# Performance work log

Measured on AMD Instinct MI355X. Metric: run time of the kernel, lower is better.

## Reference

```python
import jax, jax.numpy as jnp
import numpy as np

N = 64
K_CHEB = 5
EPS = 1e-5

# db4 decomposition filters (scaling_filter.mat Lo_D / Hi_D, length 8)
_LO = np.array([-0.010597401784997278, 0.032883011666982945, 0.030841381835986965,
                -0.18703481171888114, -0.02798376941698385, 0.6308807679295904,
                0.7148465705525415, 0.23037781330885523], dtype=np.float32)
_HI = np.array([-0.23037781330885523, 0.7148465705525415, -0.6308807679295904,
                -0.02798376941698385, 0.18703481171888114, 0.030841381835986965,
                0.032883011666982945, -0.010597401784997278], dtype=np.float32)
# torch stores np.flip(filters) and Conv2d does cross-correlation -> use flipped taps here too
_KERN = np.stack([_LO[::-1], _HI[::-1]])[:, None, None, :].copy()  # [2,1,1,8]


def _wavelet_step(x):
    # x: [B, C, 1, W]; circular pad 3 each side, depthwise len-8 conv, stride 2
    p = 3  # filter_length // 2 - 1
    xp = jnp.concatenate([x[..., -p:], x, x[..., :p]], axis=-1)
    b, c, h, wp = xp.shape
    out = jax.lax.conv_general_dilated(
        xp.reshape(b * c, 1, h, wp), jnp.asarray(_KERN), (1, 2), 'VALID',
        dimension_numbers=('NCHW', 'OIHW', 'NCHW'))
    out = out.reshape(b, c, 2, h, -1)
    return out[:, :, 0], out[:, :, 1]  # (approx, detail)


def _cbam(x, fc1, fc2, sa_w):
    # x: [B, 657, 1, 64]; channel attention then spatial attention
    def mlp(v):  # v: [B, C, 1, 1]
        h = jax.nn.relu(jnp.einsum('oc,bchw->bohw', fc1, v))
        return jnp.einsum('oc,bchw->bohw', fc2, h)
    avg = x.mean(axis=(2, 3), keepdims=True)
    mx = x.max(axis=(2, 3), keepdims=True)
    x = x * jax.nn.sigmoid(mlp(avg) + mlp(mx))
    s = jnp.concatenate([x.mean(axis=1, keepdims=True), x.max(axis=1, keepdims=True)], axis=1)
    sa = jax.nn.sigmoid(jax.lax.conv_general_dilated(
        s, sa_w, (1, 1), ((3, 3), (3, 3)), dimension_numbers=('NCHW', 'OIHW', 'NCHW')))
    return x * sa


def _global_edge_weight(w_tril, mask):
    xs, ys = np.tril_indices(N)
    E = jnp.zeros((N, N), w_tril.dtype).at[xs, ys].set(w_tril)
    E = E + E.T - jnp.diag(jnp.diag(E))
    return (E * mask).reshape(-1)


def _norm_adj(edges, w):
    # PyG NewSGConv.norm: add remaining self-loops (fill=1), deg from |w|, sym normalize
    row, col = edges[0], edges[1]
    has_self = jnp.zeros((N,), w.dtype).at[row].add(jnp.where(row == col, 1.0, 0.0)) > 0
    w_self = jnp.where(has_self, 0.0, 1.0).astype(w.dtype)
    deg = jnp.zeros((N,), w.dtype).at[row].add(jnp.abs(w)) + w_self
    dsafe = jnp.where(deg > 0, deg, 1.0)
    dinv = jnp.where(deg > 0, jax.lax.rsqrt(dsafe), 0.0)
    norm = dinv[row] * w * dinv[col]
    A = jnp.zeros((N, N), w.dtype).at[col, row].add(norm)  # out[i] = sum_j A[i,j] x[j]
    return A + jnp.diag(dinv * w_self * dinv)


def _gcn_block(x, A, W, b, g, be):
    # x: [B, N, C_in]; K-hop SGConv propagation, linear, train-mode batchnorm over (B, N)
    for _ in range(K_CHEB):
        x = jnp.einsum('ij,bjc->bic', A, x)
    x = x @ W.T + b
    mean = x.mean(axis=(0, 1))
    var = x.var(axis=(0, 1))
    return (x - mean) * jax.lax.rsqrt(var + EPS) * g + be


def _classify(x, W1, b1, g, be, W2, b2):
    out = x.reshape(x.shape[0], -1) @ W1.T + b1
    out = (out - out.mean(0)) * jax.lax.rsqrt(out.var(0) + EPS) * g + be
    return jax.nn.log_softmax(out @ W2.T + b2, axis=1)


def _forward(x, local_graph_weight, global_mask, ca_fc1, ca_fc2, sa_conv, edge_weight_tril,
             ld_W, ld_b, ld_g, ld_be, ld1_W, ld1_b, ld1_g, ld1_be,
             d_W, d_b, d_g, d_be, d1_W, d1_b, d1_g, d1_be,
             cls_W1, cls_b1, cls_g, cls_be, cls_W2, cls_b2, edges):
    xc = jnp.transpose(x, (0, 3, 2, 1))        # [B, 657, 1, 64]
    xc = _cbam(xc, ca_fc1, ca_fc2, sa_conv)
    xh = jnp.transpose(xc, (0, 3, 2, 1))       # [B, 64, 1, 657]
    # fi = floor(log2(200)) = 7 -> 4 decomposition levels: 657->328->164->82->41
    out1, _gamma = _wavelet_step(xh)
    out2, _beta = _wavelet_step(out1)
    out3, _alpha = _wavelet_step(out2)
    delta, _theta = _wavelet_step(out3)        # [B, 64, 1, 41]
    delta = delta[:, :, 0, :]                  # squeeze -> [B, 64, 41]
    gw = _global_edge_weight(edge_weight_tril, global_mask)
    A_loc = _norm_adj(edges, local_graph_weight)
    A_glb = _norm_adj(edges, gw)
    lf = _gcn_block(delta, A_loc, ld_W, ld_b, ld_g, ld_be)
    lf = _gcn_block(lf, A_loc, ld1_W, ld1_b, ld1_g, ld1_be)
    gf = _gcn_block(delta, A_glb, d_W, d_b, d_g, d_be)
    gf = _gcn_block(gf, A_glb, d1_W, d1_b, d1_g, d1_be)
    feat = jnp.concatenate([lf.mean(-1, keepdims=True), gf.mean(-1, keepdims=True)], axis=2)  # [B,64,2]
    return _classify(feat, cls_W1, cls_b1, cls_g, cls_be, cls_W2, cls_b2)


def setup_inputs() -> dict:
    key = jax.random.key(0)
    ks = iter(jax.random.split(key, 16))
    B = 512
    f32 = jnp.float32
    def rn(shape, s=0.05):
        return jax.random.normal(next(ks), shape, f32) * s
    ii = jnp.arange(N, dtype=jnp.int32)
    edges = jnp.stack([jnp.repeat(ii, N), jnp.tile(ii, N)])  # full 64x64 mesh (incl. self loops)
    return dict(
        x=jax.random.normal(next(ks), (B, N, 1, 657), f32),
        local_graph_weight=jax.random.uniform(next(ks), (N * N,), f32),
        global_mask=jnp.ones((N, N), f32),
        ca_fc1=rn((82, 657)),
        ca_fc2=rn((657, 82)),
        sa_conv=rn((1, 2, 7, 7), 0.1),
        edge_weight_tril=jax.random.uniform(next(ks), (N * (N + 1) // 2,), f32),
        ld_W=rn((16, 41)), ld_b=jnp.zeros(16, f32), ld_g=jnp.ones(16, f32), ld_be=jnp.zeros(16, f32),
        ld1_W=rn((4, 16)), ld1_b=jnp.zeros(4, f32), ld1_g=jnp.ones(4, f32), ld1_be=jnp.zeros(4, f32),
        d_W=rn((16, 41)), d_b=jnp.zeros(16, f32), d_g=jnp.ones(16, f32), d_be=jnp.zeros(16, f32),
        d1_W=rn((4, 16)), d1_b=jnp.zeros(4, f32), d1_g=jnp.ones(4, f32), d1_be=jnp.zeros(4, f32),
        cls_W1=rn((32, 128)), cls_b1=jnp.zeros(32, f32), cls_g=jnp.ones(32, f32), cls_be=jnp.zeros(32, f32),
        cls_W2=rn((2, 32)), cls_b2=jnp.zeros(2, f32),
        edges=edges,
    )


def reference(x, local_graph_weight, global_mask, ca_fc1, ca_fc2, sa_conv, edge_weight_tril,
              ld_W, ld_b, ld_g, ld_be, ld1_W, ld1_b, ld1_g, ld1_be,
              d_W, d_b, d_g, d_be, d1_W, d1_b, d1_g, d1_be,
              cls_W1, cls_b1, cls_g, cls_be, cls_W2, cls_b2, edges):
    return _forward(x, local_graph_weight, global_mask, ca_fc1, ca_fc2, sa_conv, edge_weight_tril,
                    ld_W, ld_b, ld_g, ld_be, ld1_W, ld1_b, ld1_g, ld1_be,
                    d_W, d_b, d_g, d_be, d1_W, d1_b, d1_g, d1_be,
                    cls_W1, cls_b1, cls_g, cls_be, cls_W2, cls_b2, edges)
```

## Files before the change

kernel.cpp:

```cpp
#include <hip/hip_runtime.h>
#include <math.h>

#define NB 512
#define NN 64
#define TL 657
#define LV1 328
#define LV2 164
#define LV3 82
#define LV4 41
#define HID 82
#define ST 66
#define NGB 32

#define WS_M      0
#define WS_ACC    32768
#define WS_SMEAN  36864
#define WS_SMAX   167936
#define WS_CSP    299008
#define WS_CMP    2990080
#define WS_CATT   5681152
#define WS_DELTA  299008
#define WS_Y1     5681152
#define WS_Y2     299008
#define WS_OUT1   1347584

#define ACC_Y1 0
#define ACC_Y2 64
#define ACC_O1 80

__device__ __forceinline__ float sigmoidf_(float v){ return 1.0f/(1.0f+expf(-v)); }

__device__ __forceinline__ void wav_level(float* __restrict__ dst, const float* __restrict__ src,
                                          int outL, int inL, int lane){
  const float DLO[8] = {0.23037781330885523f, 0.7148465705525415f, 0.6308807679295904f,
                        -0.02798376941698385f, -0.18703481171888114f, 0.030841381835986965f,
                        0.032883011666982945f, -0.010597401784997278f};
  for (int k=lane; k<outL; k+=64){
    int i0 = 2*k - 3;
    float a = 0.f;
    #pragma unroll
    for (int j=0;j<8;j++){
      int idx = i0 + j;
      idx = (idx < 0) ? idx + inL : ((idx >= inL) ? idx - inL : idx);
      a += src[idx]*DLO[j];
    }
    dst[k] = a;
  }
}

__global__ __launch_bounds__(512) void k_stats(
    const float* __restrict__ x,
    const float* __restrict__ lgw, const float* __restrict__ gmask,
    const float* __restrict__ tril, const int* __restrict__ edges,
    float* __restrict__ csum_p, float* __restrict__ cmax_p,
    float* __restrict__ Mout, double* __restrict__ acc)
{
  __shared__ float smem[8848];
  __shared__ float deg[64], hsv[64], dinv[64], wself[64];
  int tid = threadIdx.x;
  int bid = blockIdx.x;

  if (bid < NGB){
    int g  = bid >> 4;
    int s4 = (bid & 15) * 4;
    float* Wbuf = smem;
    float* Amat = smem + 4096;
    float* Rc   = smem + 8320;
    float* Rn   = smem + 8584;
    if (bid==0 && tid<512) acc[tid]=0.0;
    for (int e=tid;e<4096;e+=512){
      float w;
      if (g==0) w = lgw[e];
      else {
        int i=e>>6, j=e&63;
        int aa = (i>j)? i:j, bb = (i>j)? j:i;
        w = tril[aa*(aa+1)/2 + bb] * gmask[e];
      }
      Wbuf[e] = w;
    }
    for (int i=tid;i<NN*ST;i+=512) Amat[i] = 0.f;
    if (tid<64){ deg[tid]=0.f; hsv[tid]=0.f; }
    __syncthreads();
    {
      int e0 = tid*8;
      int runr = edges[e0];
      float runv = 0.f;
      #pragma unroll
      for (int i=0;i<8;i++){
        int e = e0+i;
        int r = edges[e];
        int c = edges[4096+e];
        float w = Wbuf[e];
        if (r != runr){ atomicAdd(&deg[runr], runv); runr = r; runv = 0.f; }
        runv += fabsf(w);
        if (r == c) hsv[r] = 1.f;
      }
      atomicAdd(&deg[runr], runv);
    }
    __syncthreads();
    if (tid<64){
      float w_ = (hsv[tid] > 0.f) ? 0.f : 1.f;
      float d = deg[tid] + w_;
      dinv[tid] = (d > 0.f) ? rsqrtf(d) : 0.f;
      wself[tid] = w_;
    }
    __syncthreads();
    for (int e=tid;e<4096;e+=512){
      int r = edges[e], c = edges[4096+e];
      float nm = dinv[r]*Wbuf[e]*dinv[c];
      atomicAdd(&Amat[c*ST+r], nm);
    }
    __syncthreads();
    if (tid<64) Amat[tid*ST+tid] += dinv[tid]*wself[tid]*dinv[tid];
    __syncthreads();
    if (tid < 256){
      int r = tid>>6, c = tid&63;
      Rc[r*ST+c] = Amat[(s4+r)*ST+c];
    }
    __syncthreads();
    #pragma unroll
    for (int it=0; it<4; it++){
      if (tid < 256){
        int r = tid>>6, c = tid&63;
        const float* rr = &Rc[r*ST];
        float a0=0.f, a1=0.f;
        #pragma unroll 8
        for (int k=0;k<64;k+=2){
          a0 += rr[k]  *Amat[k*ST+c];
          a1 += rr[k+1]*Amat[(k+1)*ST+c];
        }
        Rn[r*ST+c] = a0+a1;
      }
      __syncthreads();
      float* t = Rc; Rc = Rn; Rn = t;
    }
    if (tid < 256){
      int r = tid>>6, c = tid&63;
      Mout[g*4096 + (s4+r)*64 + c] = Rc[r*ST+c];
    }
    return;
  }

  int sid = bid - NGB;
  int b = sid >> 1, split = sid & 1;
  const float4* xb4 = (const float4*)(x + (size_t)b*NN*TL) + (size_t)split*8*657;
  int f0 = tid;
  int f1 = 512 + tid;
  bool has1 = (f1 < 657);
  float4 S0 = make_float4(0.f,0.f,0.f,0.f);
  float4 M0 = make_float4(-INFINITY,-INFINITY,-INFINITY,-INFINITY);
  float4 S1 = S0, M1 = M0;
  #pragma unroll
  for (int g=0; g<8; ++g){
    float4 v = xb4[g*657 + f0];
    S0.x += v.x; S0.y += v.y; S0.z += v.z; S0.w += v.w;
    M0.x = fmaxf(M0.x, v.x); M0.y = fmaxf(M0.y, v.y);
    M0.z = fmaxf(M0.z, v.z); M0.w = fmaxf(M0.w, v.w);
    if (has1){
      float4 w = xb4[g*657 + f1];
      S1.x += w.x; S1.y += w.y; S1.z += w.z; S1.w += w.w;
      M1.x = fmaxf(M1.x, w.x); M1.y = fmaxf(M1.y, w.y);
      M1.z = fmaxf(M1.z, w.z); M1.w = fmaxf(M1.w, w.w);
    }
  }
  float* Sf = smem;
  float* Mf = smem + 2628;
  *(float4*)&Sf[4*f0] = S0;
  *(float4*)&Mf[4*f0] = M0;
  if (has1){
    *(float4*)&Sf[4*f1] = S1;
    *(float4*)&Mf[4*f1] = M1;
  }
  __syncthreads();
  for (int c=tid; c<TL; c+=512){
    float s = (Sf[c] + Sf[c+657]) + (Sf[c+1314] + Sf[c+1971]);
    float m = fmaxf(fmaxf(Mf[c], Mf[c+657]), fmaxf(Mf[c+1314], Mf[c+1971]));
    csum_p[(size_t)sid*TL + c] = s;
    cmax_p[(size_t)sid*TL + c] = m;
  }
}

__global__ __launch_bounds__(512) void k_mlp(
    const float* __restrict__ csum_p, const float* __restrict__ cmax_p,
    const float* __restrict__ fc1, const float* __restrict__ fc2,
    float* __restrict__ catt_g)
{
  __shared__ float cs[660], cm[660], h[84];
  int tid = threadIdx.x, b = blockIdx.x;
  int wv = tid>>6, lane = tid&63;
  const float* s0 = csum_p + (size_t)(2*b  )*TL;
  const float* s1 = csum_p + (size_t)(2*b+1)*TL;
  const float* m0 = cmax_p + (size_t)(2*b  )*TL;
  const float* m1 = cmax_p + (size_t)(2*b+1)*TL;
  for (int c=tid; c<TL; c+=512){
    cs[c] = s0[c] + s1[c];
    cm[c] = fmaxf(m0[c], m1[c]);
  }
  __syncthreads();
  for (int o=wv; o<HID; o+=8){
    const float* fr = fc1 + (size_t)o*TL;
    float a = 0.f, bm = 0.f;
    #pragma unroll
    for (int i=0;i<11;i++){
      int c = lane + 64*i;
      if (c < TL){
        float f = fr[c];
        a += f*cs[c]; bm += f*cm[c];
      }
    }
    #pragma unroll
    for (int off=32;off;off>>=1){
      a  += __shfl_xor(a,off);
      bm += __shfl_xor(bm,off);
    }
    if (lane==0)
      h[o] = fmaxf(a*(1.0f/64.0f),0.f) + fmaxf(bm,0.f);
  }
  __syncthreads();
  for (int c=tid; c<TL; c+=512){
    const float2* fr = (const float2*)(fc2 + (size_t)c*HID);
    float a0=0.f, a1=0.f;
    #pragma unroll
    for (int u2=0;u2<41;u2++){
      float2 v = fr[u2];
      a0 += v.x*h[2*u2]; a1 += v.y*h[2*u2+1];
    }
    catt_g[(size_t)b*TL + c] = sigmoidf_(a0+a1);
  }
}

__global__ __launch_bounds__(256) void k_wav(
    const float* __restrict__ x, const float* __restrict__ catt_g,
    float* __restrict__ delta, float* __restrict__ smean, float* __restrict__ smax)
{
  __shared__ float catt[660];
  __shared__ float buf[2664];
  __shared__ float o1b[4][332];
  __shared__ float o2b[4][166];
  __shared__ float o3b[4][84];
  int tid = threadIdx.x, b = blockIdx.x, q = blockIdx.y;
  for (int i=tid;i<TL;i+=256) catt[i] = catt_g[(size_t)b*TL + i];
  __syncthreads();
  const float4* g4 = (const float4*)(x + ((size_t)b*NN + q*4)*TL);
  for (int f=tid; f<657; f+=256){
    float4 v = g4[f];
    int e = 4*f;
    if (f==164 || f==328 || f==492){
      float ev[4] = {v.x, v.y, v.z, v.w};
      #pragma unroll
      for (int j=0;j<4;j++){
        int ee = e+j;
        int r = (ee>=657) + (ee>=1314) + (ee>=1971);
        buf[ee + 12*r] = ev[j];
      }
    } else {
      int r = (e>=657) + (e>=1314) + (e>=1971);
      *(float4*)&buf[e + 12*r] = v;
    }
  }
  __syncthreads();
  int wv = tid>>6, lane = tid&63;
  int n = q*4 + wv;
  float* y = &buf[669*wv];
  float ls = 0.f, lm = -INFINITY;
  #pragma unroll
  for (int i=0;i<11;i++){
    int t = lane + 64*i;
    if (t < TL){
      float vv = y[t]*catt[t];
      y[t] = vv; ls += vv; lm = fmaxf(lm,vv);
    }
  }
  #pragma unroll
  for (int off=32;off;off>>=1){
    ls += __shfl_xor(ls,off);
    lm = fmaxf(lm, __shfl_xor(lm,off));
  }
  if (lane==0){ smean[b*NN+n] = ls*(1.0f/657.0f); smax[b*NN+n] = lm; }
  wav_level(o1b[wv], y,       LV1, TL,  lane);
  wav_level(o2b[wv], o1b[wv], LV2, LV1, lane);
  wav_level(o3b[wv], o2b[wv], LV3, LV2, lane);
  if (lane < LV4){
    const float DLO[8] = {0.23037781330885523f, 0.7148465705525415f, 0.6308807679295904f,
                          -0.02798376941698385f, -0.18703481171888114f, 0.030841381835986965f,
                          0.032883011666982945f, -0.010597401784997278f};
    int i0 = 2*lane - 3;
    float a = 0.f;
    #pragma unroll
    for (int j=0;j<8;j++){
      int idx = i0 + j;
      idx = (idx < 0) ? idx + LV3 : ((idx >= LV3) ? idx - LV3 : idx);
      a += o3b[wv][idx]*DLO[j];
    }
    delta[((size_t)b*NN + n)*LV4 + lane] = a;
  }
}

__global__ __launch_bounds__(256) void k_gcn1(
  const float* __restrict__ delta, const float* __restrict__ Mmat,
  const float* __restrict__ smean, const float* __restrict__ smax,
  const float* __restrict__ saw,
  const float* __restrict__ ldW, const float* __restrict__ ldb,
  const float* __restrict__ dW, const float* __restrict__ db2,
  float* __restrict__ Y1, double* __restrict__ acc)
{
  __shared__ float Dl[NN*LV4];
  __shared__ float Tt[NN*16];
  __shared__ float Mm[4096];
  __shared__ float Wl[16*LV4];
  __shared__ float satt[NN];
  __shared__ double red[256];
  int tid=threadIdx.x, b=blockIdx.x;
  if (tid < NN){
    float a = 0.f;
    #pragma unroll
    for (int kw=0;kw<7;kw++){
      int w = tid + kw - 3;
      if (0<=w && w<NN) a += smean[b*NN+w]*saw[21+kw] + smax[b*NN+w]*saw[70+kw];
    }
    satt[tid] = sigmoidf_(a);
  }
  __syncthreads();
  const float* ds = delta + (size_t)b*NN*LV4;
  for (int i=tid;i<NN*LV4;i+=256) Dl[i] = ds[i]*satt[i/LV4];
  for (int g=0; g<2; g++){
    const float* Ws = g ? dW : ldW;
    const float* bs = g ? db2 : ldb;
    for (int i=tid;i<16*LV4;i+=256) Wl[i]=Ws[i];
    const float4* Mm4 = (const float4*)(Mmat + g*4096);
    for (int i=tid;i<1024;i+=256) *(float4*)&Mm[4*i] = Mm4[i];
    __syncthreads();
    for (int e=tid;e<NN*16;e+=256){
      int n=e>>4, o=e&15;
      const float* dr=&Dl[n*LV4];
      const float* wr=&Wl[o*LV4];
      float a=0.f;
      #pragma unroll 8
      for (int c=0;c<LV4;c++) a += dr[c]*wr[c];
      Tt[e]=a;
    }
    __syncthreads();
    float bias = bs[tid&15];
    float ps=0.f, pq=0.f;
    for (int m=0;m<4;m++){
      int e=tid+256*m;
      int n=e>>4, o=e&15;
      float a=bias;
      #pragma unroll 8
      for (int k=0;k<64;k++) a += Mm[n*64+k]*Tt[k*16+o];
      Y1[((size_t)b*NN+n)*32 + g*16 + o] = a;
      ps += a; pq += a*a;
    }
    red[tid]=(double)ps;
    __syncthreads();
    if (tid<16){ double t=0; for (int r=tid;r<256;r+=16) t+=red[r]; atomicAdd(&acc[ACC_Y1+g*32+tid], t); }
    __syncthreads();
    red[tid]=(double)pq;
    __syncthreads();
    if (tid<16){ double t=0; for (int r=tid;r<256;r+=16) t+=red[r]; atomicAdd(&acc[ACC_Y1+g*32+16+tid], t); }
    __syncthreads();
  }
}

__global__ __launch_bounds__(256) void k_gcn2(
  const float* __restrict__ Y1, const float* __restrict__ Mmat,
  const float* __restrict__ ldg, const float* __restrict__ ldbe,
  const float* __restrict__ dg, const float* __restrict__ dbe,
  const float* __restrict__ ld1W, const float* __restrict__ ld1b,
  const float* __restrict__ d1W, const float* __restrict__ d1b,
  float* __restrict__ Y2, double* __restrict__ acc)
{
  __shared__ float Yl[NN*32];
  __shared__ float T2[NN*8];
  __shared__ float Mm[2*4096];
  __shared__ float scl[32], sht[32];
  __shared__ double red[256];
  int tid=threadIdx.x, b=blockIdx.x;
  const float4* ys4 = (const float4*)(Y1 + (size_t)b*NN*32);
  for (int i=tid;i<512;i+=256) *(float4*)&Yl[4*i] = ys4[i];
  const float4* Mm4 = (const float4*)Mmat;
  for (int i=tid;i<2048;i+=256) *(float4*)&Mm[4*i] = Mm4[i];
  if (tid<32){
    int g=tid>>4, o=tid&15;
    double s=acc[ACC_Y1+g*32+o], q=acc[ACC_Y1+g*32+16+o];
    double mean=s/32768.0;
    double var=q/32768.0 - mean*mean;
    float gam = g? dg[o] : ldg[o];
    float bet = g? dbe[o] : ldbe[o];
    float sc = gam * rsqrtf((float)var + 1e-5f);
    scl[tid]=sc; sht[tid]=bet - (float)mean*sc;
  }
  __syncthreads();
  for (int i=tid;i<NN*32;i+=256){ int c=i&31; Yl[i]=Yl[i]*scl[c]+sht[c]; }
  __syncthreads();
  for (int e=tid;e<NN*8;e+=256){
    int n=e>>3, c=e&7, g=c>>2, p=c&3;
    const float* w = (g? d1W : ld1W) + p*16;
    const float* yr = &Yl[n*32 + g*16];
    float a=0.f;
    #pragma unroll
    for (int o=0;o<16;o++) a += yr[o]*w[o];
    T2[e]=a;
  }
  __syncthreads();
  float ps=0.f,pq=0.f;
  for (int m=0;m<2;m++){
    int e=tid+256*m;
    int n=e>>3, c=e&7, g=c>>2;
    float a = g? d1b[c&3] : ld1b[c&3];
    const float* mr=&Mm[g*4096+n*64];
    #pragma unroll 8
    for (int k=0;k<64;k++) a += mr[k]*T2[k*8+c];
    Y2[((size_t)b*NN+n)*8 + c] = a;
    ps+=a; pq+=a*a;
  }
  red[tid]=(double)ps; __syncthreads();
  if (tid<8){ double t=0; for (int r=tid;r<256;r+=8) t+=red[r]; atomicAdd(&acc[ACC_Y2 + (tid>>2)*8 + (tid&3)], t); }
  __syncthreads();
  red[tid]=(double)pq; __syncthreads();
  if (tid<8){ double t=0; for (int r=tid;r<256;r+=8) t+=red[r]; atomicAdd(&acc[ACC_Y2 + (tid>>2)*8 + 4 + (tid&3)], t); }
}

__global__ __launch_bounds__(64) void k_featcls(
  const float* __restrict__ Y2,
  const float* __restrict__ ld1g, const float* __restrict__ ld1be,
  const float* __restrict__ d1g, const float* __restrict__ d1be,
  const float* __restrict__ W1, const float* __restrict__ b1,
  float* __restrict__ out1, double* __restrict__ acc)
{
  __shared__ float f[128];
  __shared__ float scl[8], sht[8];
  int tid=threadIdx.x, b=blockIdx.x;
  if (tid<8){
    int g=tid>>2, p=tid&3;
    double s=acc[ACC_Y2+g*8+p], q=acc[ACC_Y2+g*8+4+p];
    double mean=s/32768.0;
    double var=q/32768.0-mean*mean;
    float gam = g? d1g[p]:ld1g[p];
    float bet = g? d1be[p]:ld1be[p];
    float sc = gam*rsqrtf((float)var+1e-5f);
    scl[tid]=sc; sht[tid]=bet-(float)mean*sc;
  }
  __syncthreads();
  {
    const float* yr = Y2 + ((size_t)b*NN+tid)*8;
    float lf=0.f, gf=0.f;
    #pragma unroll
    for (int p=0;p<4;p++){
      lf += yr[p]*scl[p]+sht[p];
      gf += yr[4+p]*scl[4+p]+sht[4+p];
    }
    f[2*tid]   = lf*0.25f;
    f[2*tid+1] = gf*0.25f;
  }
  __syncthreads();
  if (tid<32){
    const float* w = W1 + tid*128;
    float a = b1[tid];
    #pragma unroll 4
    for (int m=0;m<128;m++) a += w[m]*f[m];
    out1[b*32+tid]=a;
    atomicAdd(&acc[ACC_O1+tid], (double)a);
    atomicAdd(&acc[ACC_O1+32+tid], (double)(a*a));
  }
}

__global__ __launch_bounds__(64) void k_cls2(
  const float* __restrict__ out1,
  const float* __restrict__ cg, const float* __restrict__ cbe,
  const float* __restrict__ W2, const float* __restrict__ b2,
  const double* __restrict__ acc, float* __restrict__ out)
{
  __shared__ float v[32];
  __shared__ float z[2];
  int tid=threadIdx.x, b=blockIdx.x;
  if (tid<32){
    double s=acc[ACC_O1+tid], q=acc[ACC_O1+32+tid];
    double mean=s/512.0;
    double var=q/512.0-mean*mean;
    float sc=cg[tid]*rsqrtf((float)var+1e-5f);
    float sh=cbe[tid]-(float)mean*sc;
    v[tid]=out1[b*32+tid]*sc+sh;
  }
  __syncthreads();
  if (tid<2){
    const float* w=W2+tid*32;
    float a=b2[tid];
    #pragma unroll
    for (int j=0;j<32;j++) a += w[j]*v[j];
    z[tid]=a;
  }
  __syncthreads();
  if (tid<2){
    float m=fmaxf(z[0],z[1]);
    float l=m+logf(expf(z[0]-m)+expf(z[1]-m));
    out[b*2+tid]=z[tid]-l;
  }
}

extern "C" void kernel_launch(void* const* d_in, const int* in_sizes, int n_in,
                              void* d_out, int out_size, void* d_ws, size_t ws_size,
                              hipStream_t stream) {
  (void)in_sizes; (void)n_in; (void)out_size; (void)ws_size;
  const float* x     = (const float*)d_in[0];
  const float* lgw   = (const float*)d_in[1];
  const float* gmask = (const float*)d_in[2];
  const float* fc1   = (const float*)d_in[3];
  const float* fc2   = (const float*)d_in[4];
  const float* saw   = (const float*)d_in[5];
  const float* tril  = (const float*)d_in[6];
  const float* ldW   = (const float*)d_in[7];
  const float* ldb   = (const float*)d_in[8];
  const float* ldg   = (const float*)d_in[9];
  const float* ldbe  = (const float*)d_in[10];
  const float* ld1W  = (const float*)d_in[11];
  const float* ld1b  = (const float*)d_in[12];
  const float* ld1g  = (const float*)d_in[13];
  const float* ld1be = (const float*)d_in[14];
  const float* dW    = (const float*)d_in[15];
  const float* db2   = (const float*)d_in[16];
  const float* dg    = (const float*)d_in[17];
  const float* dbe   = (const float*)d_in[18];
  const float* d1W   = (const float*)d_in[19];
  const float* d1b   = (const float*)d_in[20];
  const float* d1g   = (const float*)d_in[21];
  const float* d1be  = (const float*)d_in[22];
  const float* cW1   = (const float*)d_in[23];
  const float* cb1   = (const float*)d_in[24];
  const float* cgam  = (const float*)d_in[25];
  const float* cbet  = (const float*)d_in[26];
  const float* cW2   = (const float*)d_in[27];
  const float* cb2   = (const float*)d_in[28];
  const int*   edges = (const int*)d_in[29];

  char* ws = (char*)d_ws;
  float*  M      = (float*)(ws + WS_M);
  double* acc    = (double*)(ws + WS_ACC);
  float*  smean  = (float*)(ws + WS_SMEAN);
  float*  smax   = (float*)(ws + WS_SMAX);
  float*  csum_p = (float*)(ws + WS_CSP);
  float*  cmax_p = (float*)(ws + WS_CMP);
  float*  catt   = (float*)(ws + WS_CATT);
  float*  delta  = (float*)(ws + WS_DELTA);
  float*  Y1     = (float*)(ws + WS_Y1);
  float*  Y2     = (float*)(ws + WS_Y2);
  float*  out1   = (float*)(ws + WS_OUT1);
  float*  out    = (float*)d_out;

  k_stats<<<NGB + 2*NB, 512, 0, stream>>>(x, lgw, gmask, tril, edges,
                                          csum_p, cmax_p, M, acc);
  k_mlp<<<NB, 512, 0, stream>>>(csum_p, cmax_p, fc1, fc2, catt);
  k_wav<<<dim3(NB, 16), 256, 0, stream>>>(x, catt, delta, smean, smax);
  k_gcn1<<<NB, 256, 0, stream>>>(delta, M, smean, smax, saw, ldW, ldb, dW, db2, Y1, acc);
  k_gcn2<<<NB, 256, 0, stream>>>(Y1, M, ldg, ldbe, dg, dbe, ld1W, ld1b, d1W, d1b, Y2, acc);
  k_featcls<<<NB, 64, 0, stream>>>(Y2, ld1g, ld1be, d1g, d1be, cW1, cb1, out1, acc);
  k_cls2<<<NB, 64, 0, stream>>>(out1, cgam, cbet, cW2, cb2, acc, out);
}
```

Baseline: 168.7 us.

## Fuse GCN and classifier tail kernels into one cooperative kernel with grid syncs

Merges the four tail kernels (gcn1, gcn2, feature classifier, cls2) into a single cooperative kernel. Batch-norm statistics are gathered across the grid with grid.sync(), and the intermediate activations stay in shared memory instead of going through global workspace. This removes three launches and the global round-trips for Y1, Y2 and out1. In exchange it needs all 512 blocks co-resident for the cooperative launch, and grid syncs have their own cost.

```diff
diff --git a/kernel.cpp b/kernel.cpp
--- a/kernel.cpp
+++ b/kernel.cpp
@@ -1,5 +1,8 @@
 #include <hip/hip_runtime.h>
+#include <hip/hip_cooperative_groups.h>
 #include <math.h>
+
+namespace cg = cooperative_groups;
 
 #define NB 512
 #define NN 64
@@ -19,10 +22,7 @@
 #define WS_CSP    299008
 #define WS_CMP    2990080
 #define WS_CATT   5681152
-#define WS_DELTA  299008
-#define WS_Y1     5681152
-#define WS_Y2     299008
-#define WS_OUT1   1347584
+#define WS_DELTA  7026688
 
 #define ACC_Y1 0
 #define ACC_Y2 64
@@ -296,21 +296,36 @@
   }
 }
 
-__global__ __launch_bounds__(256) void k_gcn1(
+__global__ __launch_bounds__(256) void k_tail(
   const float* __restrict__ delta, const float* __restrict__ Mmat,
   const float* __restrict__ smean, const float* __restrict__ smax,
   const float* __restrict__ saw,
   const float* __restrict__ ldW, const float* __restrict__ ldb,
   const float* __restrict__ dW, const float* __restrict__ db2,
-  float* __restrict__ Y1, double* __restrict__ acc)
+  const float* __restrict__ ldg, const float* __restrict__ ldbe,
+  const float* __restrict__ dg, const float* __restrict__ dbe,
+  const float* __restrict__ ld1W, const float* __restrict__ ld1b,
+  const float* __restrict__ d1W, const float* __restrict__ d1b,
+  const float* __restrict__ ld1g, const float* __restrict__ ld1be,
+  const float* __restrict__ d1g, const float* __restrict__ d1be,
+  const float* __restrict__ cW1, const float* __restrict__ cb1,
+  const float* __restrict__ cgam, const float* __restrict__ cbet,
+  const float* __restrict__ cW2, const float* __restrict__ cb2,
+  double* __restrict__ acc, float* __restrict__ out)
 {
+  cg::grid_group grid = cg::this_grid();
+  __shared__ float Yl[NN*32];
+  __shared__ float Y2l[NN*8];
+  __shared__ float o1l[32];
   __shared__ float Dl[NN*LV4];
-  __shared__ float Tt[NN*16];
   __shared__ float Mm[4096];
+  __shared__ float Tt[1024];
   __shared__ float Wl[16*LV4];
   __shared__ float satt[NN];
+  __shared__ float scl[32], sht[32];
   __shared__ double red[256];
-  int tid=threadIdx.x, b=blockIdx.x;
+  int tid = threadIdx.x, b = blockIdx.x;
+
   if (tid < NN){
     float a = 0.f;
     #pragma unroll
@@ -348,7 +363,7 @@
       float a=bias;
       #pragma unroll 8
       for (int k=0;k<64;k++) a += Mm[n*64+k]*Tt[k*16+o];
-      Y1[((size_t)b*NN+n)*32 + g*16 + o] = a;
+      Yl[n*32 + g*16 + o] = a;
       ps += a; pq += a*a;
     }
     red[tid]=(double)ps;
@@ -360,26 +375,9 @@
     if (tid<16){ double t=0; for (int r=tid;r<256;r+=16) t+=red[r]; atomicAdd(&acc[ACC_Y1+g*32+16+tid], t); }
     __syncthreads();
   }
-}
-
-__global__ __launch_bounds__(256) void k_gcn2(
-  const float* __restrict__ Y1, const float* __restrict__ Mmat,
-  const float* __restrict__ ldg, const float* __restrict__ ldbe,
-  const float* __restrict__ dg, const float* __restrict__ dbe,
-  const float* __restrict__ ld1W, const float* __restrict__ ld1b,
-  const float* __restrict__ d1W, const float* __restrict__ d1b,
-  float* __restrict__ Y2, double* __restrict__ acc)
-{
-  __shared__ float Yl[NN*32];
-  __shared__ float T2[NN*8];
-  __shared__ float Mm[2*4096];
-  __shared__ float scl[32], sht[32];
-  __shared__ double red[256];
-  int tid=threadIdx.x, b=blockIdx.x;
-  const float4* ys4 = (const float4*)(Y1 + (size_t)b*NN*32);
-  for (int i=tid;i<512;i+=256) *(float4*)&Yl[4*i] = ys4[i];
-  const float4* Mm4 = (const float4*)Mmat;
-  for (int i=tid;i<2048;i+=256) *(float4*)&Mm[4*i] = Mm4[i];
+
+  grid.sync();
+
   if (tid<32){
     int g=tid>>4, o=tid&15;
     double s=acc[ACC_Y1+g*32+o], q=acc[ACC_Y1+g*32+16+o];
@@ -400,37 +398,31 @@
     float a=0.f;
     #pragma unroll
     for (int o=0;o<16;o++) a += yr[o]*w[o];
-    T2[e]=a;
-  }
-  __syncthreads();
-  float ps=0.f,pq=0.f;
-  for (int m=0;m<2;m++){
-    int e=tid+256*m;
-    int n=e>>3, c=e&7, g=c>>2;
-    float a = g? d1b[c&3] : ld1b[c&3];
-    const float* mr=&Mm[g*4096+n*64];
+    Tt[e]=a;
+  }
+  __syncthreads();
+  for (int g=0; g<2; g++){
+    const float4* Mm4 = (const float4*)(Mmat + g*4096);
+    for (int i=tid;i<1024;i+=256) *(float4*)&Mm[4*i] = Mm4[i];
+    __syncthreads();
+    int n = tid>>2, p = tid&3, c = g*4+p;
+    float a = g? d1b[p] : ld1b[p];
+    const float* mr = &Mm[n*64];
     #pragma unroll 8
-    for (int k=0;k<64;k++) a += mr[k]*T2[k*8+c];
-    Y2[((size_t)b*NN+n)*8 + c] = a;
-    ps+=a; pq+=a*a;
-  }
-  red[tid]=(double)ps; __syncthreads();
-  if (tid<8){ double t=0; for (int r=tid;r<256;r+=8) t+=red[r]; atomicAdd(&acc[ACC_Y2 + (tid>>2)*8 + (tid&3)], t); }
-  __syncthreads();
-  red[tid]=(double)pq; __syncthreads();
-  if (tid<8){ double t=0; for (int r=tid;r<256;r+=8) t+=red[r]; atomicAdd(&acc[ACC_Y2 + (tid>>2)*8 + 4 + (tid&3)], t); }
-}
-
-__global__ __launch_bounds__(64) void k_featcls(
-  const float* __restrict__ Y2,
-  const float* __restrict__ ld1g, const float* __restrict__ ld1be,
-  const float* __restrict__ d1g, const float* __restrict__ d1be,
-  const float* __restrict__ W1, const float* __restrict__ b1,
-  float* __restrict__ out1, double* __restrict__ acc)
-{
-  __shared__ float f[128];
-  __shared__ float scl[8], sht[8];
-  int tid=threadIdx.x, b=blockIdx.x;
+    for (int k=0;k<64;k++) a += mr[k]*Tt[k*8+c];
+    Y2l[n*8+c] = a;
+    red[tid]=(double)a;
+    __syncthreads();
+    if (tid<4){ double t=0; for (int r=tid;r<256;r+=4) t+=red[r]; atomicAdd(&acc[ACC_Y2+g*8+tid], t); }
+    __syncthreads();
+    red[tid]=(double)(a*a);
+    __syncthreads();
+    if (tid<4){ double t=0; for (int r=tid;r<256;r+=4) t+=red[r]; atomicAdd(&acc[ACC_Y2+g*8+4+tid], t); }
+    __syncthreads();
+  }
+
+  grid.sync();
+
   if (tid<8){
     int g=tid>>2, p=tid&3;
     double s=acc[ACC_Y2+g*8+p], q=acc[ACC_Y2+g*8+4+p];
@@ -442,59 +434,51 @@
     scl[tid]=sc; sht[tid]=bet-(float)mean*sc;
   }
   __syncthreads();
-  {
-    const float* yr = Y2 + ((size_t)b*NN+tid)*8;
+  if (tid < NN){
+    const float* yr = &Y2l[tid*8];
     float lf=0.f, gf=0.f;
     #pragma unroll
     for (int p=0;p<4;p++){
       lf += yr[p]*scl[p]+sht[p];
       gf += yr[4+p]*scl[4+p]+sht[4+p];
     }
-    f[2*tid]   = lf*0.25f;
-    f[2*tid+1] = gf*0.25f;
+    Tt[2*tid]   = lf*0.25f;
+    Tt[2*tid+1] = gf*0.25f;
   }
   __syncthreads();
   if (tid<32){
-    const float* w = W1 + tid*128;
-    float a = b1[tid];
+    const float* w = cW1 + tid*128;
+    float a = cb1[tid];
     #pragma unroll 4
-    for (int m=0;m<128;m++) a += w[m]*f[m];
-    out1[b*32+tid]=a;
+    for (int m=0;m<128;m++) a += w[m]*Tt[m];
+    o1l[tid]=a;
     atomicAdd(&acc[ACC_O1+tid], (double)a);
     atomicAdd(&acc[ACC_O1+32+tid], (double)(a*a));
   }
-}
-
-__global__ __launch_bounds__(64) void k_cls2(
-  const float* __restrict__ out1,
-  const float* __restrict__ cg, const float* __restrict__ cbe,
-  const float* __restrict__ W2, const float* __restrict__ b2,
-  const double* __restrict__ acc, float* __restrict__ out)
-{
-  __shared__ float v[32];
-  __shared__ float z[2];
-  int tid=threadIdx.x, b=blockIdx.x;
+
+  grid.sync();
+
   if (tid<32){
     double s=acc[ACC_O1+tid], q=acc[ACC_O1+32+tid];
     double mean=s/512.0;
     double var=q/512.0-mean*mean;
-    float sc=cg[tid]*rsqrtf((float)var+1e-5f);
-    float sh=cbe[tid]-(float)mean*sc;
-    v[tid]=out1[b*32+tid]*sc+sh;
+    float sc=cgam[tid]*rsqrtf((float)var+1e-5f);
+    float sh=cbet[tid]-(float)mean*sc;
+    Tt[tid]=o1l[tid]*sc+sh;
   }
   __syncthreads();
   if (tid<2){
-    const float* w=W2+tid*32;
-    float a=b2[tid];
-    #pragma unroll
-    for (int j=0;j<32;j++) a += w[j]*v[j];
-    z[tid]=a;
+    const float* w=cW2+tid*32;
+    float a=cb2[tid];
+    #pragma unroll
+    for (int j=0;j<32;j++) a += w[j]*Tt[j];
+    Tt[64+tid]=a;
   }
   __syncthreads();
   if (tid<2){
-    float m=fmaxf(z[0],z[1]);
-    float l=m+logf(expf(z[0]-m)+expf(z[1]-m));
-    out[b*2+tid]=z[tid]-l;
+    float m=fmaxf(Tt[64],Tt[65]);
+    float l=m+logf(expf(Tt[64]-m)+expf(Tt[65]-m));
+    out[b*2+tid]=Tt[64+tid]-l;
   }
 }
 
@@ -542,17 +526,21 @@
   float*  cmax_p = (float*)(ws + WS_CMP);
   float*  catt   = (float*)(ws + WS_CATT);
   float*  delta  = (float*)(ws + WS_DELTA);
-  float*  Y1     = (float*)(ws + WS_Y1);
-  float*  Y2     = (float*)(ws + WS_Y2);
-  float*  out1   = (float*)(ws + WS_OUT1);
   float*  out    = (float*)d_out;
 
   k_stats<<<NGB + 2*NB, 512, 0, stream>>>(x, lgw, gmask, tril, edges,
                                           csum_p, cmax_p, M, acc);
   k_mlp<<<NB, 512, 0, stream>>>(csum_p, cmax_p, fc1, fc2, catt);
   k_wav<<<dim3(NB, 16), 256, 0, stream>>>(x, catt, delta, smean, smax);
-  k_gcn1<<<NB, 256, 0, stream>>>(delta, M, smean, smax, saw, ldW, ldb, dW, db2, Y1, acc);
-  k_gcn2<<<NB, 256, 0, stream>>>(Y1, M, ldg, ldbe, dg, dbe, ld1W, ld1b, d1W, d1b, Y2, acc);
-  k_featcls<<<NB, 64, 0, stream>>>(Y2, ld1g, ld1be, d1g, d1be, cW1, cb1, out1, acc);
-  k_cls2<<<NB, 64, 0, stream>>>(out1, cgam, cbet, cW2, cb2, acc, out);
+
+  void* args[] = {
+    (void*)&delta, (void*)&M, (void*)&smean, (void*)&smax, (void*)&saw,
+    (void*)&ldW, (void*)&ldb, (void*)&dW, (void*)&db2,
+    (void*)&ldg, (void*)&ldbe, (void*)&dg, (void*)&dbe,
+    (void*)&ld1W, (void*)&ld1b, (void*)&d1W, (void*)&d1b,
+    (void*)&ld1g, (void*)&ld1be, (void*)&d1g, (void*)&d1be,
+    (void*)&cW1, (void*)&cb1, (void*)&cgam, (void*)&cbet,
+    (void*)&cW2, (void*)&cb2, (void*)&acc, (void*)&out
+  };
+  hipLaunchCooperativeKernel((void*)k_tail, dim3(NB), dim3(256), args, 0, stream);
 }
```

New measurement: 297.0 us. +76.0%, slower.
